# Performance work log

Measured on AMD Instinct MI355X. Metric: run time of the kernel, lower is better.

## Reference

```python
import jax, jax.numpy as jnp
import numpy as np

NUM_EMBEDDINGS = 1024
EMBEDDING_DIM = 64
COMMITMENT_COST = 0.25


def setup_inputs() -> dict:
    key = jax.random.key(0)
    k1, k2 = jax.random.split(key)
    inputs = jax.random.normal(k1, (64, 2048, EMBEDDING_DIM), dtype=jnp.float32)
    # matches torch init: uniform(-1/K, 1/K)
    codebook = jax.random.uniform(
        k2, (NUM_EMBEDDINGS, EMBEDDING_DIM), dtype=jnp.float32,
        minval=-1.0 / NUM_EMBEDDINGS, maxval=1.0 / NUM_EMBEDDINGS)
    return {"inputs": inputs, "codebook": codebook}


def reference(inputs, codebook):
    orig_shape = inputs.shape
    flat = inputs.reshape(-1, EMBEDDING_DIM)            # [N, D]
    # squared Euclidean distances (same argmin as torch.cdist)
    d2 = (jnp.sum(flat * flat, axis=1, keepdims=True)   # [N, 1]
          - 2.0 * flat @ codebook.T                      # [N, K]
          + jnp.sum(codebook * codebook, axis=1)[None, :])
    encoding_indices = jnp.argmin(d2, axis=1)            # [N] int
    quantized = codebook[encoding_indices].reshape(orig_shape)

    e_latent_loss = jnp.mean((jax.lax.stop_gradient(quantized) - inputs) ** 2)
    q_latent_loss = jnp.mean((quantized - jax.lax.stop_gradient(inputs)) ** 2)
    loss = q_latent_loss + COMMITMENT_COST * e_latent_loss

    # straight-through estimator
    quantized_ste = inputs + jax.lax.stop_gradient(quantized - inputs)
    return quantized_ste, loss, encoding_indices
```

## Files before the change

### kernel.cpp

```cpp
#include <hip/hip_runtime.h>


#define NROWS  131072
#define DIM    64
#define KCB    1024
#define QSIZE  (NROWS * DIM)

typedef unsigned long long u64;
typedef unsigned int u32;
typedef unsigned short ushortx;
typedef __attribute__((ext_vector_type(8))) short short8v;
typedef __attribute__((ext_vector_type(4))) float f32x4;

__device__ __forceinline__ u32 umin32(u32 a, u32 b) { return a < b ? a : b; }
__device__ __forceinline__ u32 umax32(u32 a, u32 b) { return a > b ? a : b; }

__device__ __forceinline__ ushortx f2bf(float f) {
    u32 u = __float_as_uint(f);
    u32 r = u + 0x7FFFu + ((u >> 16) & 1u);
    return (ushortx)(r >> 16);
}
__device__ __forceinline__ float bf2f(ushortx h) {
    return __uint_as_float(((u32)h) << 16);
}

__global__ __launch_bounds__(256) void vq_prep(const float* __restrict__ cb,
                                               float* __restrict__ csq,
                                               float* __restrict__ cs18b,
                                               ushortx* __restrict__ cbsw,
                                               float* __restrict__ loss_slot) {
    int k = blockIdx.x * 256 + threadIdx.x;
    if (k < KCB) {
        const float* c = cb + k * DIM;
        float a0 = 0.f, a1 = 0.f, a2 = 0.f, a3 = 0.f;
        #pragma unroll
        for (int d = 0; d < 16; ++d) {
            a0 = fmaf(c[d],      c[d],      a0);
            a1 = fmaf(c[16 + d], c[16 + d], a1);
            a2 = fmaf(c[32 + d], c[32 + d], a2);
            a3 = fmaf(c[48 + d], c[48 + d], a3);
        }
        const float cs = (a0 + a1) + (a2 + a3);
        csq[k] = cs;
        cs18b[k] = cs * 262144.0f + 131072.0f;

        const int ct = k >> 4;
        const int j  = k & 15;
        #pragma unroll
        for (int q = 0; q < 4; ++q) {
            const int L = q * 16 + j;
            #pragma unroll
            for (int h = 0; h < 2; ++h) {
                union { ushortx u[8]; short8v v; } uh, ul;
                #pragma unroll
                for (int e = 0; e < 8; ++e) {
                    const float f = c[h * 32 + q * 8 + e];
                    const ushortx hh = f2bf(f);
                    uh.u[e] = hh;
                    ul.u[e] = f2bf(f - bf2f(hh));
                }
                *reinterpret_cast<short8v*>(cbsw + ct * 2048 + h * 512 + L * 8) = uh.v;
                *reinterpret_cast<short8v*>(cbsw + ct * 2048 + 1024 + h * 512 + L * 8) = ul.v;
            }
        }
    }
    if (blockIdx.x == 0 && threadIdx.x == 0) *loss_slot = 0.f;
}

__global__ __launch_bounds__(256, 4) void vq_main(const float* __restrict__ x,
                                                  const float* __restrict__ cb,
                                                  const float* __restrict__ csq,
                                                  const float* __restrict__ cs18b,
                                                  const ushortx* __restrict__ cbsw,
                                                  float* __restrict__ out_q,
                                                  float* __restrict__ out_loss,
                                                  float* __restrict__ out_idx) {
    __shared__ u32   sTop[4][32][3];
    __shared__ int   sFinal[128];
    __shared__ float sLoss[4];

    const int tid  = threadIdx.x;
    const int lane = tid & 63;
    const int wid  = tid >> 6;
    const size_t rowbase = (size_t)blockIdx.x * 128;
    const int wrow0 = wid * 32;
    const int lcol  = lane & 15;
    const int lkq   = lane >> 4;

    short8v Ah[2][2], Al[2][2];
    #pragma unroll
    for (int t = 0; t < 2; ++t)
        #pragma unroll
        for (int h = 0; h < 2; ++h) {
            const float* xp = x + (rowbase + (size_t)(wrow0 + t * 16 + lcol)) * DIM
                              + h * 32 + lkq * 8;
            const float4 u0 = *reinterpret_cast<const float4*>(xp);
            const float4 u1 = *reinterpret_cast<const float4*>(xp + 4);
            const float xv[8] = {u0.x, u0.y, u0.z, u0.w, u1.x, u1.y, u1.z, u1.w};
            union { ushortx u[8]; short8v v; } uh, ul;
            #pragma unroll
            for (int j = 0; j < 8; ++j) {
                const ushortx hh = f2bf(xv[j]);
                uh.u[j] = hh;
                ul.u[j] = f2bf(xv[j] - bf2f(hh));
            }
            Ah[t][h] = uh.v;
            Al[t][h] = ul.v;
        }

    u32 k1[8], k2[8], k3[8];
    #pragma unroll
    for (int s = 0; s < 8; ++s) { k1[s] = ~0u; k2[s] = ~0u; k3[s] = ~0u; }

    u32 nlane = (u32)lcol;
    const ushortx* bp = cbsw + (size_t)lane * 8;

    #pragma unroll 1
    for (int ct = 0; ct < 64; ++ct) {
        const short8v Bh0 = *reinterpret_cast<const short8v*>(bp);
        const short8v Bh1 = *reinterpret_cast<const short8v*>(bp + 512);
        const short8v Bl0 = *reinterpret_cast<const short8v*>(bp + 1024);
        const short8v Bl1 = *reinterpret_cast<const short8v*>(bp + 1536);
        const float csb = cs18b[nlane];
        #pragma unroll
        for (int t = 0; t < 2; ++t) {
            f32x4 acc = (f32x4){0.f, 0.f, 0.f, 0.f};
            acc = __builtin_amdgcn_mfma_f32_16x16x32_bf16(Ah[t][0], Bh0, acc, 0, 0, 0);
            acc = __builtin_amdgcn_mfma_f32_16x16x32_bf16(Al[t][0], Bh0, acc, 0, 0, 0);
            acc = __builtin_amdgcn_mfma_f32_16x16x32_bf16(Ah[t][0], Bl0, acc, 0, 0, 0);
            acc = __builtin_amdgcn_mfma_f32_16x16x32_bf16(Ah[t][1], Bh1, acc, 0, 0, 0);
            acc = __builtin_amdgcn_mfma_f32_16x16x32_bf16(Al[t][1], Bh1, acc, 0, 0, 0);
            acc = __builtin_amdgcn_mfma_f32_16x16x32_bf16(Ah[t][1], Bl1, acc, 0, 0, 0);
            #pragma unroll
            for (int r = 0; r < 4; ++r) {
                const float m18 = fmaf(acc[r], -524288.0f, csb);
                const u32 key = ((u32)m18 << 10) | nlane;
                const int s = t * 4 + r;
                const u32 nk1 = umin32(key, k1[s]);
                const u32 mx  = umax32(key, k1[s]);
                const u32 nk2 = umin32(k2[s], mx);
                const u32 mx2 = umax32(k2[s], mx);
                k3[s] = umin32(k3[s], mx2);
                k1[s] = nk1; k2[s] = nk2;
            }
        }
        bp += 2048; nlane += 16;
    }

    #pragma unroll
    for (int s = 0; s < 8; ++s) {
        u32 a1 = k1[s], a2 = k2[s], a3 = k3[s];
        #pragma unroll
        for (int mask = 1; mask <= 8; mask <<= 1) {
            const u32 b1 = __shfl_xor(a1, mask, 64);
            const u32 b2 = __shfl_xor(a2, mask, 64);
            const u32 b3 = __shfl_xor(a3, mask, 64);
            const u32 c1 = umin32(a1, b1), d1 = umax32(a1, b1);
            const u32 c2 = umin32(a2, b2);
            const u32 o3 = umin32(umax32(d1, c2), umin32(a3, b3));
            a1 = c1; a2 = umin32(d1, c2); a3 = o3;
        }
        k1[s] = a1; k2[s] = a2; k3[s] = a3;
    }
    if (lcol < 8) {
        const int j = lcol, g = lkq;
        const int row = (j >> 2) * 16 + g * 4 + (j & 3);
        sTop[wid][row][0] = k1[j]; sTop[wid][row][1] = k2[j]; sTop[wid][row][2] = k3[j];
    }
    __syncthreads();

    if (lane < 32) {
        const int row = wrow0 + lane;
        const u32 K1 = sTop[wid][lane][0];
        const u32 K2 = sTop[wid][lane][1];
        const u32 K3 = sTop[wid][lane][2];
        int idx = (int)(K1 & 1023u);
        const u32 m1q = K1 >> 10, m2q = K2 >> 10;
        if (m2q - m1q <= 26u) {
            const float* xr = x + (rowbase + (size_t)row) * DIM;
            float4 xv[16];
            #pragma unroll
            for (int q = 0; q < 16; ++q) xv[q] = reinterpret_cast<const float4*>(xr)[q];
            float p[4];
            #pragma unroll
            for (int q = 0; q < 4; ++q) {
                float a = 0.f;
                #pragma unroll
                for (int e = 0; e < 4; ++e) {
                    const float4 v = xv[4 * q + e];
                    a = fmaf(v.x, v.x, a); a = fmaf(v.y, v.y, a);
                    a = fmaf(v.z, v.z, a); a = fmaf(v.w, v.w, a);
                }
                p[q] = a;
            }
            const float asq = (p[0] + p[1]) + (p[2] + p[3]);
            const u32 Mq = (u32)fmaf(asq, 0.126f, 5.0f);
            u64 best = ~0ull;
            #pragma unroll 1
            for (int c = 0; c < 3; ++c) {
                const u32 Kc = c == 0 ? K1 : (c == 1 ? K2 : K3);
                const u32 mq = Kc >> 10;
                if (c > 0 && (mq - m1q) > Mq) break;
                const int n = (int)(Kc & 1023u);
                const float4* cr = reinterpret_cast<const float4*>(cb + (size_t)n * DIM);
                float acc = 0.f;
                #pragma unroll
                for (int q = 0; q < 16; ++q) {
                    const float4 c4 = cr[q], v = xv[q];
                    acc = fmaf(v.x, c4.x, acc); acc = fmaf(v.y, c4.y, acc);
                    acc = fmaf(v.z, c4.z, acc); acc = fmaf(v.w, c4.w, acc);
                }
                const float tt = asq - 2.0f * acc;
                const float dd = tt + csq[n];
                const u64 kk = ((u64)__float_as_uint(dd) << 32) | (u32)n;
                best = kk < best ? kk : best;
            }
            idx = (int)(u32)best;
        }
        sFinal[row] = idx;
        out_idx[rowbase + row] = (float)idx;
    }
    __syncthreads();

    #pragma unroll 1
    for (int sub = 0; sub < 2; ++sub) {
        const size_t base = (rowbase + 64 * sub) * DIM;
        float lsum = 0.f;
        #pragma unroll 4
        for (int i = tid; i < 64 * DIM; i += 256) {
            const int r = i >> 6;
            const int d = i & 63;
            const int kb = sFinal[64 * sub + r];
            const float q  = cb[(size_t)kb * DIM + d];
            const float xe = x[base + i];
            out_q[base + i] = xe + (q - xe);
            const float df = q - xe;
            lsum = fmaf(df, df, lsum);
        }
        #pragma unroll
        for (int off = 32; off; off >>= 1) lsum += __shfl_down(lsum, off, 64);
        if (lane == 0) sLoss[wid] = lsum;
        __syncthreads();
        if (tid == 0) {
            const float tot = (sLoss[0] + sLoss[1]) + (sLoss[2] + sLoss[3]);
            atomicAdd(out_loss, tot * (1.25f / 8388608.0f));
        }
        __syncthreads();
    }
}

extern "C" void kernel_launch(void* const* d_in, const int* in_sizes, int n_in,
                              void* d_out, int out_size, void* d_ws, size_t ws_size,
                              hipStream_t stream) {
    const float* x  = (const float*)d_in[0];
    const float* cb = (const float*)d_in[1];
    float* out      = (float*)d_out;
    float* out_loss = out + QSIZE;
    float* out_idx  = out + QSIZE + 1;

    float*   csq   = (float*)d_ws;
    float*   cs18b = csq + 1024;
    ushortx* cbsw  = (ushortx*)(csq + 2048);

    vq_prep<<<4, 256, 0, stream>>>(cb, csq, cs18b, cbsw, out_loss);
    vq_main<<<NROWS / 128, 256, 0, stream>>>(x, cb, csq, cs18b, cbsw,
                                             out, out_loss, out_idx);
}
```

Before: 160.4 us.

## Prefetch codebook tiles, fold scale and bias into MFMA, widen prep kernel

The main loop now loads the next codebook tile's bf16 fragments and bias one iteration ahead, so the loads overlap the MFMA work. The -2*2^18 scale is folded into the bf16 split of the codebook and the bias is used to initialise the accumulator, which removes one fma per output element. Because scaling before the split changes rounding, the rescore thresholds are widened, which sends more rows through the exact fp32 recheck. The prep kernel spreads each codebook row over four threads. The last iteration reads past the end of the codebook buffers, and the wider margins add rescore work.

```diff
diff --git a/kernel.cpp b/kernel.cpp
--- a/kernel.cpp
+++ b/kernel.cpp
@@ -29,42 +29,44 @@
                                                float* __restrict__ cs18b,
                                                ushortx* __restrict__ cbsw,
                                                float* __restrict__ loss_slot) {
-    int k = blockIdx.x * 256 + threadIdx.x;
-    if (k < KCB) {
-        const float* c = cb + k * DIM;
-        float a0 = 0.f, a1 = 0.f, a2 = 0.f, a3 = 0.f;
-        #pragma unroll
-        for (int d = 0; d < 16; ++d) {
-            a0 = fmaf(c[d],      c[d],      a0);
-            a1 = fmaf(c[16 + d], c[16 + d], a1);
-            a2 = fmaf(c[32 + d], c[32 + d], a2);
-            a3 = fmaf(c[48 + d], c[48 + d], a3);
-        }
-        const float cs = (a0 + a1) + (a2 + a3);
-        csq[k] = cs;
-        cs18b[k] = cs * 262144.0f + 131072.0f;
-
-        const int ct = k >> 4;
-        const int j  = k & 15;
-        #pragma unroll
-        for (int q = 0; q < 4; ++q) {
-            const int L = q * 16 + j;
-            #pragma unroll
-            for (int h = 0; h < 2; ++h) {
-                union { ushortx u[8]; short8v v; } uh, ul;
-                #pragma unroll
-                for (int e = 0; e < 8; ++e) {
-                    const float f = c[h * 32 + q * 8 + e];
-                    const ushortx hh = f2bf(f);
-                    uh.u[e] = hh;
-                    ul.u[e] = f2bf(f - bf2f(hh));
-                }
-                *reinterpret_cast<short8v*>(cbsw + ct * 2048 + h * 512 + L * 8) = uh.v;
-                *reinterpret_cast<short8v*>(cbsw + ct * 2048 + 1024 + h * 512 + L * 8) = ul.v;
-            }
-        }
-    }
-    if (blockIdx.x == 0 && threadIdx.x == 0) *loss_slot = 0.f;
+    const int gid = blockIdx.x * 256 + threadIdx.x;
+    const int k  = gid >> 2;
+    const int qt = gid & 3;
+    const float* c = cb + k * DIM;
+
+    float aq = 0.f;
+    #pragma unroll
+    for (int d = 0; d < 16; ++d) {
+        const float v = c[16 * qt + d];
+        aq = fmaf(v, v, aq);
+    }
+    const float s1 = aq + __shfl_xor(aq, 1, 64);
+    const float s2 = s1 + __shfl_xor(s1, 2, 64);
+    if (qt == 0) {
+        csq[k]   = s2;
+        cs18b[k] = s2 * 262144.0f + 131072.0f;
+    }
+
+    const int ct = k >> 4;
+    const int j  = k & 15;
+    #pragma unroll
+    for (int cc = 0; cc < 2; ++cc) {
+        const int c8 = 2 * qt + cc;
+        const int h  = c8 >> 2;
+        const int qq = c8 & 3;
+        const int L  = qq * 16 + j;
+        union { ushortx u[8]; short8v v; } uh, ul;
+        #pragma unroll
+        for (int e = 0; e < 8; ++e) {
+            const float g = c[c8 * 8 + e] * -524288.0f;
+            const ushortx hh = f2bf(g);
+            uh.u[e] = hh;
+            ul.u[e] = f2bf(g - bf2f(hh));
+        }
+        *reinterpret_cast<short8v*>(cbsw + ct * 2048 + h * 512 + L * 8) = uh.v;
+        *reinterpret_cast<short8v*>(cbsw + ct * 2048 + 1024 + h * 512 + L * 8) = ul.v;
+    }
+    if (gid == 0) *loss_slot = 0.f;
 }
 
 __global__ __launch_bounds__(256, 4) void vq_main(const float* __restrict__ x,
@@ -115,16 +117,26 @@
     u32 nlane = (u32)lcol;
     const ushortx* bp = cbsw + (size_t)lane * 8;
 
+    short8v pBh0 = *reinterpret_cast<const short8v*>(bp);
+    short8v pBh1 = *reinterpret_cast<const short8v*>(bp + 512);
+    short8v pBl0 = *reinterpret_cast<const short8v*>(bp + 1024);
+    short8v pBl1 = *reinterpret_cast<const short8v*>(bp + 1536);
+    float   pcs  = cs18b[nlane];
+
     #pragma unroll 1
     for (int ct = 0; ct < 64; ++ct) {
-        const short8v Bh0 = *reinterpret_cast<const short8v*>(bp);
-        const short8v Bh1 = *reinterpret_cast<const short8v*>(bp + 512);
-        const short8v Bl0 = *reinterpret_cast<const short8v*>(bp + 1024);
-        const short8v Bl1 = *reinterpret_cast<const short8v*>(bp + 1536);
-        const float csb = cs18b[nlane];
+        const short8v Bh0 = pBh0, Bh1 = pBh1, Bl0 = pBl0, Bl1 = pBl1;
+        const float csb = pcs;
+        bp += 2048;
+        pBh0 = *reinterpret_cast<const short8v*>(bp);
+        pBh1 = *reinterpret_cast<const short8v*>(bp + 512);
+        pBl0 = *reinterpret_cast<const short8v*>(bp + 1024);
+        pBl1 = *reinterpret_cast<const short8v*>(bp + 1536);
+        pcs  = cs18b[nlane + 16];
+
         #pragma unroll
         for (int t = 0; t < 2; ++t) {
-            f32x4 acc = (f32x4){0.f, 0.f, 0.f, 0.f};
+            f32x4 acc = (f32x4){csb, csb, csb, csb};
             acc = __builtin_amdgcn_mfma_f32_16x16x32_bf16(Ah[t][0], Bh0, acc, 0, 0, 0);
             acc = __builtin_amdgcn_mfma_f32_16x16x32_bf16(Al[t][0], Bh0, acc, 0, 0, 0);
             acc = __builtin_amdgcn_mfma_f32_16x16x32_bf16(Ah[t][0], Bl0, acc, 0, 0, 0);
@@ -133,8 +145,7 @@
             acc = __builtin_amdgcn_mfma_f32_16x16x32_bf16(Ah[t][1], Bl1, acc, 0, 0, 0);
             #pragma unroll
             for (int r = 0; r < 4; ++r) {
-                const float m18 = fmaf(acc[r], -524288.0f, csb);
-                const u32 key = ((u32)m18 << 10) | nlane;
+                const u32 key = ((u32)acc[r] << 10) | nlane;
                 const int s = t * 4 + r;
                 const u32 nk1 = umin32(key, k1[s]);
                 const u32 mx  = umax32(key, k1[s]);
@@ -144,7 +155,7 @@
                 k1[s] = nk1; k2[s] = nk2;
             }
         }
-        bp += 2048; nlane += 16;
+        nlane += 16;
     }
 
     #pragma unroll
@@ -176,7 +187,7 @@
         const u32 K3 = sTop[wid][lane][2];
         int idx = (int)(K1 & 1023u);
         const u32 m1q = K1 >> 10, m2q = K2 >> 10;
-        if (m2q - m1q <= 26u) {
+        if (m2q - m1q <= 48u) {
             const float* xr = x + (rowbase + (size_t)row) * DIM;
             float4 xv[16];
             #pragma unroll
@@ -194,7 +205,7 @@
                 p[q] = a;
             }
             const float asq = (p[0] + p[1]) + (p[2] + p[3]);
-            const u32 Mq = (u32)fmaf(asq, 0.126f, 5.0f);
+            const u32 Mq = (u32)fmaf(asq, 0.126f, 24.0f);
             u64 best = ~0ull;
             #pragma unroll 1
             for (int c = 0; c < 3; ++c) {
@@ -262,7 +273,7 @@
     float*   cs18b = csq + 1024;
     ushortx* cbsw  = (ushortx*)(csq + 2048);
 
-    vq_prep<<<4, 256, 0, stream>>>(cb, csq, cs18b, cbsw, out_loss);
+    vq_prep<<<16, 256, 0, stream>>>(cb, csq, cs18b, cbsw, out_loss);
     vq_main<<<NROWS / 128, 256, 0, stream>>>(x, cb, csq, cs18b, cbsw,
                                              out, out_loss, out_idx);
 }
```

Measured after the change: 161.6 us. About the same (+0.7%).
